# Kernel optimization log

Measured on AMD Instinct MI355X. Metric: run time of the kernel, lower is better.

## Reference

```python
import jax, jax.numpy as jnp
import numpy as np

HEADS = 12
HEAD_DIM = 64          # dim_out // heads = 768 // 12
Q_STRIDE = 4
WINDOW_SIZE = 16       # post-pool tokens per window; pre-pool = Q_STRIDE*WINDOW_SIZE = 64
DIM = 768
DIM_OUT = 768


def setup_inputs() -> dict:
    key = jax.random.key(0)
    k1, k2, k3 = jax.random.split(key, 3)
    B, N = 32, 3136
    x = jax.random.normal(k1, (B, N, DIM), dtype=jnp.float32)
    Wqkv = jax.random.normal(k2, (DIM, 3 * DIM_OUT), dtype=jnp.float32) * 0.02
    bqkv = jnp.zeros((3 * DIM_OUT,), dtype=jnp.float32)
    Wproj = jax.random.normal(k3, (DIM_OUT, DIM_OUT), dtype=jnp.float32) * 0.02
    bproj = jnp.zeros((DIM_OUT,), dtype=jnp.float32)
    return {"x": x, "Wqkv": Wqkv, "bqkv": bqkv, "Wproj": Wproj, "bproj": bproj}


def reference(x, Wqkv, bqkv, Wproj, bproj):
    B, N, _ = x.shape
    num_windows = N // (Q_STRIDE * WINDOW_SIZE)  # 49
    scale = HEAD_DIM ** (-0.5)

    # QKV projection (torch Linear uses x @ W^T; here Wqkv is stored [dim, 3*dim_out])
    qkv = x @ Wqkv + bqkv                                  # [B, N, 3*dim_out]
    # Same reshape as torch: windows are the inner split of the token axis
    qkv = qkv.reshape(B, N // num_windows, num_windows, 3, HEADS, HEAD_DIM)
    qkv = jnp.transpose(qkv, (3, 0, 4, 2, 1, 5))           # [3, B, h, w, t, d]
    q, k, v = qkv[0], qkv[1], qkv[2]                       # t = Q_STRIDE*WINDOW_SIZE

    # Query max-pooling over stride groups
    q = q.reshape(B, HEADS, num_windows, Q_STRIDE, WINDOW_SIZE, HEAD_DIM).max(axis=3)
    # q: [B, h, w, WINDOW_SIZE, d]

    # Scaled dot-product attention within each window
    logits = jnp.einsum('bhwqd,bhwkd->bhwqk', q, k) * scale
    attn = jax.nn.softmax(logits, axis=-1)
    o = jnp.einsum('bhwqk,bhwkd->bhwqd', attn, v)          # [B, h, w, q, d]

    # transpose(1,3) then flatten tokens, channels = heads*head_dim
    o = jnp.transpose(o, (0, 3, 2, 1, 4)).reshape(B, -1, DIM_OUT)
    return o @ Wproj + bproj
```

## Files before the change

kernel.cpp:

```cpp
#include <hip/hip_runtime.h>
#include <hip/hip_bf16.h>


typedef __bf16 bf16x8 __attribute__((ext_vector_type(8)));
typedef float f32x4 __attribute__((ext_vector_type(4)));
typedef unsigned short u16x8 __attribute__((ext_vector_type(8)));

#define GLOBAL_AS __attribute__((address_space(1)))
#define LDS_AS __attribute__((address_space(3)))

__device__ __forceinline__ unsigned short f2bf(float f) {
    unsigned u = __builtin_bit_cast(unsigned, f);
    u += 0x7FFFu + ((u >> 16) & 1u);
    return (unsigned short)(u >> 16);
}
__device__ __forceinline__ float bf2f(unsigned short h) {
    return __builtin_bit_cast(float, (unsigned)h << 16);
}

__device__ __forceinline__ void load16_to_lds(const void* g, void* l) {
    __builtin_amdgcn_global_load_lds((const GLOBAL_AS unsigned int*)g,
                                     (LDS_AS unsigned int*)l, 16, 0, 0);
}

__global__ void cvt_f32_bf16(const float* __restrict__ in,
                             unsigned short* __restrict__ out, long n4) {
    long i = (long)blockIdx.x * blockDim.x + threadIdx.x;
    if (i >= n4) return;
    float4 f = ((const float4*)in)[i];
    uint2 u;
    u.x = (unsigned)f2bf(f.x) | ((unsigned)f2bf(f.y) << 16);
    u.y = (unsigned)f2bf(f.z) | ((unsigned)f2bf(f.w) << 16);
    ((uint2*)out)[i] = u;
}

__global__ void transpose_cvt(const float* __restrict__ W,
                              unsigned short* __restrict__ Wt, int K, int N) {
    __shared__ float tile[32][33];
    int bx = blockIdx.x * 32;
    int by = blockIdx.y * 32;
    int tx = threadIdx.x & 31, ty = threadIdx.x >> 5;
    #pragma unroll
    for (int i = 0; i < 32; i += 8)
        tile[ty + i][tx] = W[(size_t)(by + ty + i) * N + bx + tx];
    __syncthreads();
    #pragma unroll
    for (int i = 0; i < 32; i += 8)
        Wt[(size_t)(bx + ty + i) * K + by + tx] = f2bf(tile[tx][ty + i]);
}

template <bool OUT_BF16>
__global__ __launch_bounds__(256)
void gemm_bt(const unsigned short* __restrict__ A,
             const unsigned short* __restrict__ Bt,
             const float* __restrict__ bias,
             void* __restrict__ Cv, int M, int N, int K) {
    __shared__ alignas(16) unsigned short lsA[128 * 64];
    __shared__ alignas(16) unsigned short lsB[128 * 64];

    const int tid  = threadIdx.x;
    const int lane = tid & 63;
    const int wave = tid >> 6;
    const int wm = (wave >> 1) * 64;
    const int wn = (wave & 1) * 64;

    const int nwg = (int)(gridDim.x * gridDim.y);
    const int hid = (int)(blockIdx.y * gridDim.x + blockIdx.x);
    int lid = hid;
    if ((nwg & 7) == 0) {
        const int cpx = nwg >> 3;
        lid = (hid & 7) * cpx + (hid >> 3);
    }
    const int tileX = lid % (int)gridDim.x;
    const int tileY = lid / (int)gridDim.x;
    const long bm = (long)tileY * 128;
    const long bn = (long)tileX * 128;

    const int arow  = tid >> 3;
    const int acolb = (((tid & 7) ^ ((tid >> 3) & 7)) * 16);
    const char* gA = (const char*)A + ((bm + arow) * (long)K) * 2 + acolb;
    const char* gB = (const char*)Bt + ((bn + arow) * (long)K) * 2 + acolb;
    const long rowStep = (long)K * 2 * 32;
    const int ldsWaveBase = wave * 512;

    f32x4 acc[4][4] = {};

    for (int kt = 0; kt < K; kt += 64) {
        #pragma unroll
        for (int it = 0; it < 4; ++it) {
            load16_to_lds(gA + it * rowStep, &lsA[it * 2048 + ldsWaveBase]);
            load16_to_lds(gB + it * rowStep, &lsB[it * 2048 + ldsWaveBase]);
        }
        gA += 128; gB += 128;
        __syncthreads();
        #pragma unroll
        for (int ks = 0; ks < 64; ks += 32) {
            bf16x8 af[4], bg[4];
            const int colSwz = (ks + ((lane >> 4) & 3) * 8) ^ ((lane & 7) * 8);
            #pragma unroll
            for (int i = 0; i < 4; ++i) {
                const int rowA = wm + i * 16 + (lane & 15);
                af[i] = *(const bf16x8*)&lsA[rowA * 64 + colSwz];
                const int rowB = wn + i * 16 + (lane & 15);
                bg[i] = *(const bf16x8*)&lsB[rowB * 64 + colSwz];
            }
            #pragma unroll
            for (int i = 0; i < 4; ++i)
                #pragma unroll
                for (int j = 0; j < 4; ++j)
                    acc[i][j] = __builtin_amdgcn_mfma_f32_16x16x32_bf16(
                        bg[j], af[i], acc[i][j], 0, 0, 0);
        }
        __syncthreads();
    }

    const int lane15 = lane & 15;
    const int quad   = lane >> 4;
    const long rbase = bm + wm + lane15;
    const int  cbase = (int)bn + wn + quad * 4;
    #pragma unroll
    for (int j = 0; j < 4; ++j) {
        const int col = cbase + j * 16;
        const float4 bv = *(const float4*)&bias[col];
        #pragma unroll
        for (int i = 0; i < 4; ++i) {
            const long row = rbase + i * 16;
            const size_t idx = (size_t)row * N + col;
            const float v0 = acc[i][j][0] + bv.x;
            const float v1 = acc[i][j][1] + bv.y;
            const float v2 = acc[i][j][2] + bv.z;
            const float v3 = acc[i][j][3] + bv.w;
            if constexpr (OUT_BF16) {
                ushort4 s;
                s.x = f2bf(v0); s.y = f2bf(v1); s.z = f2bf(v2); s.w = f2bf(v3);
                *(ushort4*)((unsigned short*)Cv + idx) = s;
            } else {
                float4 s;
                s.x = v0; s.y = v1; s.z = v2; s.w = v3;
                *(float4*)((float*)Cv + idx) = s;
            }
        }
    }
}

__global__ __launch_bounds__(256)
void attn_win_mfma(const unsigned short* __restrict__ qkv,
                   unsigned short* __restrict__ o) {
    const int hg = blockIdx.x;
    const int w  = blockIdx.y;
    const int b  = blockIdx.z;
    const int wave = threadIdx.x >> 6;
    const int lane = threadIdx.x & 63;
    const int h = hg * 4 + wave;
    const int l = lane & 15;
    const int quad = lane >> 4;

    __shared__ alignas(16) unsigned short vT[4][64 * 72];
    __shared__ alignas(16) unsigned short ps[4][16 * 72];

    const long tokStride = 49L * 2304;
    const long base = ((long)b * 3136 + w) * 2304 + h * 64;

    bf16x8 af[2];
    {
        const unsigned short* qr = qkv + base + (long)l * tokStride + quad * 8;
        float m0[8], m1[8];
        #pragma unroll
        for (int sg = 0; sg < 4; ++sg) {
            uint4 u0 = *(const uint4*)(qr + (long)sg * 16 * tokStride);
            uint4 u1 = *(const uint4*)(qr + (long)sg * 16 * tokStride + 32);
            const unsigned short* p0 = (const unsigned short*)&u0;
            const unsigned short* p1 = (const unsigned short*)&u1;
            #pragma unroll
            for (int e = 0; e < 8; ++e) {
                float f0 = bf2f(p0[e]), f1 = bf2f(p1[e]);
                if (sg == 0) { m0[e] = f0; m1[e] = f1; }
                else { m0[e] = fmaxf(m0[e], f0); m1[e] = fmaxf(m1[e], f1); }
            }
        }
        u16x8 a0, a1;
        #pragma unroll
        for (int e = 0; e < 8; ++e) {
            a0[e] = f2bf(m0[e] * 0.125f);
            a1[e] = f2bf(m1[e] * 0.125f);
        }
        af[0] = __builtin_bit_cast(bf16x8, a0);
        af[1] = __builtin_bit_cast(bf16x8, a1);
    }

    {
        const unsigned short* vr = qkv + base + (long)lane * tokStride + 1536;
        unsigned short* vw = &vT[wave][0];
        #pragma unroll
        for (int i = 0; i < 8; ++i) {
            uint4 u = *(const uint4*)(vr + i * 8);
            const unsigned short* pe = (const unsigned short*)&u;
            #pragma unroll
            for (int e = 0; e < 8; ++e)
                vw[(i * 8 + e) * 72 + lane] = pe[e];
        }
    }

    f32x4 Sc[4] = {};
    {
        bf16x8 bk0, bk1;
        #pragma unroll
        for (int tt = 0; tt < 4; ++tt) {
            const unsigned short* kr =
                qkv + base + (long)(tt * 16 + l) * tokStride + 768 + quad * 8;
            bk0 = __builtin_bit_cast(bf16x8, *(const uint4*)kr);
            bk1 = __builtin_bit_cast(bf16x8, *(const uint4*)(kr + 32));
            Sc[tt] = __builtin_amdgcn_mfma_f32_16x16x32_bf16(af[0], bk0, Sc[tt], 0, 0, 0);
            Sc[tt] = __builtin_amdgcn_mfma_f32_16x16x32_bf16(af[1], bk1, Sc[tt], 0, 0, 0);
        }
    }

    float pr[4][4];
    {
        #pragma unroll
        for (int r = 0; r < 4; ++r) {
            float mx = fmaxf(fmaxf(Sc[0][r], Sc[1][r]), fmaxf(Sc[2][r], Sc[3][r]));
            #pragma unroll
            for (int off = 1; off < 16; off <<= 1)
                mx = fmaxf(mx, __shfl_xor(mx, off));
            float sum = 0.f;
            #pragma unroll
            for (int tt = 0; tt < 4; ++tt) {
                pr[tt][r] = __expf(Sc[tt][r] - mx);
                sum += pr[tt][r];
            }
            #pragma unroll
            for (int off = 1; off < 16; off <<= 1)
                sum += __shfl_xor(sum, off);
            const float inv = 1.0f / sum;
            #pragma unroll
            for (int tt = 0; tt < 4; ++tt) pr[tt][r] *= inv;
        }
    }

    {
        unsigned short* pw = &ps[wave][0];
        #pragma unroll
        for (int r = 0; r < 4; ++r)
            #pragma unroll
            for (int tt = 0; tt < 4; ++tt)
                pw[(quad * 4 + r) * 72 + tt * 16 + l] = f2bf(pr[tt][r]);
    }

    f32x4 Oc[4] = {};
    {
        #pragma unroll
        for (int s = 0; s < 2; ++s) {
            bf16x8 ap = *(const bf16x8*)&ps[wave][l * 72 + s * 32 + quad * 8];
            #pragma unroll
            for (int tt = 0; tt < 4; ++tt) {
                bf16x8 bv = *(const bf16x8*)&vT[wave][(tt * 16 + l) * 72 + s * 32 + quad * 8];
                Oc[tt] = __builtin_amdgcn_mfma_f32_16x16x32_bf16(ap, bv, Oc[tt], 0, 0, 0);
            }
        }
    }

    {
        const long obase = ((long)b * 784 + (long)(quad * 4) * 49 + w) * 768 + h * 64 + l;
        #pragma unroll
        for (int tt = 0; tt < 4; ++tt)
            #pragma unroll
            for (int r = 0; r < 4; ++r)
                o[obase + (long)r * 49 * 768 + tt * 16] = f2bf(Oc[tt][r]);
    }
}

extern "C" void kernel_launch(void* const* d_in, const int* in_sizes, int n_in,
                              void* d_out, int out_size, void* d_ws, size_t ws_size,
                              hipStream_t stream) {
    const float* x     = (const float*)d_in[0];
    const float* Wqkv  = (const float*)d_in[1];
    const float* bqkv  = (const float*)d_in[2];
    const float* Wproj = (const float*)d_in[3];
    const float* bproj = (const float*)d_in[4];
    float* out = (float*)d_out;

    const long needed1 = (32L * 3136 * 768 + 32L * 3136 * 2304 +
                          25088L * 768 + 2304L * 768 + 768L * 768) * 2;
    const int C  = (ws_size >= (size_t)needed1) ? 1 : 4;
    const int CB = 32 / C;
    const long XC = (long)CB * 3136 * 768;
    const long QC = (long)CB * 3136 * 2304;

    char* p = (char*)d_ws;
    unsigned short* xb    = (unsigned short*)p; p += XC * 2;
    unsigned short* qkvb  = (unsigned short*)p; p += QC * 2;
    unsigned short* ob    = (unsigned short*)p; p += 25088L * 768 * 2;
    unsigned short* WqkvT = (unsigned short*)p; p += 2304L * 768 * 2;
    unsigned short* WprojT= (unsigned short*)p; p += 768L * 768 * 2;

    transpose_cvt<<<dim3(72, 24), 256, 0, stream>>>(Wqkv, WqkvT, 768, 2304);
    transpose_cvt<<<dim3(24, 24), 256, 0, stream>>>(Wproj, WprojT, 768, 768);

    const int M = CB * 3136;
    for (int c = 0; c < C; ++c) {
        cvt_f32_bf16<<<(int)(XC / 4 / 256), 256, 0, stream>>>(x + (size_t)c * XC, xb, XC / 4);
        gemm_bt<true><<<dim3(18, M / 128), 256, 0, stream>>>(
            xb, WqkvT, bqkv, qkvb, M, 2304, 768);
        attn_win_mfma<<<dim3(3, 49, CB), 256, 0, stream>>>(
            qkvb, ob + (size_t)c * CB * 784 * 768);
    }
    gemm_bt<false><<<dim3(6, 196), 256, 0, stream>>>(
        ob, WprojT, bproj, out, 25088, 768, 768);
}
```

Measured before the change: 1.230 ms.

## Enlarge GEMM tiles to 256x256 with double-buffered LDS prefetch

Both GEMMs now use 256x256 block tiles with 512 threads (8 waves, each computing 128x64) instead of 128x128 tiles with 256 threads. LDS is double-buffered so the next K-tile's global-to-LDS loads are issued while the current tile is being consumed, leaving one barrier per K step. The XCD-aware block remap now also handles grid sizes that are not multiples of 8. The larger tiles raise operand reuse and cut global traffic per FLOP. The cost is 128 KB of LDS and a 128-register accumulator per thread, which limits occupancy and leaves fewer blocks to fill the GPU.

Result: faster. 1.178 ms (-4.3%).

```diff
diff --git a/kernel.cpp b/kernel.cpp
--- a/kernel.cpp
+++ b/kernel.cpp
@@ -50,72 +50,80 @@
 }
 
 template <bool OUT_BF16>
-__global__ __launch_bounds__(256)
-void gemm_bt(const unsigned short* __restrict__ A,
-             const unsigned short* __restrict__ Bt,
-             const float* __restrict__ bias,
-             void* __restrict__ Cv, int M, int N, int K) {
-    __shared__ alignas(16) unsigned short lsA[128 * 64];
-    __shared__ alignas(16) unsigned short lsB[128 * 64];
+__global__ __launch_bounds__(512, 2)
+void gemm_bt256(const unsigned short* __restrict__ A,
+                const unsigned short* __restrict__ Bt,
+                const float* __restrict__ bias,
+                void* __restrict__ Cv, int M, int N, int K) {
+    __shared__ alignas(16) unsigned short lsA[2][256 * 64];
+    __shared__ alignas(16) unsigned short lsB[2][256 * 64];
 
     const int tid  = threadIdx.x;
     const int lane = tid & 63;
     const int wave = tid >> 6;
-    const int wm = (wave >> 1) * 64;
-    const int wn = (wave & 1) * 64;
+    const int wm = (wave >> 2) * 128;
+    const int wn = (wave & 3) * 64;
 
     const int nwg = (int)(gridDim.x * gridDim.y);
     const int hid = (int)(blockIdx.y * gridDim.x + blockIdx.x);
-    int lid = hid;
-    if ((nwg & 7) == 0) {
-        const int cpx = nwg >> 3;
-        lid = (hid & 7) * cpx + (hid >> 3);
-    }
+    const int q8  = nwg >> 3, r8 = nwg & 7;
+    const int xcd = hid & 7;
+    const int lid = (xcd < r8 ? xcd * (q8 + 1) : r8 * (q8 + 1) + (xcd - r8) * q8)
+                    + (hid >> 3);
     const int tileX = lid % (int)gridDim.x;
     const int tileY = lid / (int)gridDim.x;
-    const long bm = (long)tileY * 128;
-    const long bn = (long)tileX * 128;
+    const long bm = (long)tileY * 256;
+    const long bn = (long)tileX * 256;
 
     const int arow  = tid >> 3;
-    const int acolb = (((tid & 7) ^ ((tid >> 3) & 7)) * 16);
+    const int acolb = (((tid & 7) ^ (arow & 7)) * 16);
     const char* gA = (const char*)A + ((bm + arow) * (long)K) * 2 + acolb;
     const char* gB = (const char*)Bt + ((bn + arow) * (long)K) * 2 + acolb;
-    const long rowStep = (long)K * 2 * 32;
+    const long rowStep = (long)K * 2 * 64;
     const int ldsWaveBase = wave * 512;
 
-    f32x4 acc[4][4] = {};
-
-    for (int kt = 0; kt < K; kt += 64) {
+    f32x4 acc[8][4] = {};
+
+    const int NT = K >> 6;
+
+    auto STAGE = [&](int buf, int t) {
+        const char* a = gA + (long)t * 128;
+        const char* b = gB + (long)t * 128;
         #pragma unroll
         for (int it = 0; it < 4; ++it) {
-            load16_to_lds(gA + it * rowStep, &lsA[it * 2048 + ldsWaveBase]);
-            load16_to_lds(gB + it * rowStep, &lsB[it * 2048 + ldsWaveBase]);
-        }
-        gA += 128; gB += 128;
+            load16_to_lds(a + it * rowStep, &lsA[buf][it * 4096 + ldsWaveBase]);
+            load16_to_lds(b + it * rowStep, &lsB[buf][it * 4096 + ldsWaveBase]);
+        }
+    };
+
+    STAGE(0, 0);
+    int cur = 0;
+    const int lane15 = lane & 15;
+    const int quad   = lane >> 4;
+
+    for (int t = 0; t < NT; ++t) {
         __syncthreads();
+        if (t + 1 < NT) STAGE(cur ^ 1, t + 1);
         #pragma unroll
         for (int ks = 0; ks < 64; ks += 32) {
-            bf16x8 af[4], bg[4];
-            const int colSwz = (ks + ((lane >> 4) & 3) * 8) ^ ((lane & 7) * 8);
-            #pragma unroll
-            for (int i = 0; i < 4; ++i) {
-                const int rowA = wm + i * 16 + (lane & 15);
-                af[i] = *(const bf16x8*)&lsA[rowA * 64 + colSwz];
-                const int rowB = wn + i * 16 + (lane & 15);
-                bg[i] = *(const bf16x8*)&lsB[rowB * 64 + colSwz];
-            }
-            #pragma unroll
-            for (int i = 0; i < 4; ++i)
+            bf16x8 af[8], bg[4];
+            const int colSwz = (ks + quad * 8) ^ ((lane & 7) * 8);
+            #pragma unroll
+            for (int i = 0; i < 8; ++i)
+                af[i] = *(const bf16x8*)&lsA[cur][(wm + i * 16 + lane15) * 64 + colSwz];
+            #pragma unroll
+            for (int j = 0; j < 4; ++j)
+                bg[j] = *(const bf16x8*)&lsB[cur][(wn + j * 16 + lane15) * 64 + colSwz];
+            #pragma unroll
+            for (int i = 0; i < 8; ++i)
                 #pragma unroll
                 for (int j = 0; j < 4; ++j)
                     acc[i][j] = __builtin_amdgcn_mfma_f32_16x16x32_bf16(
                         bg[j], af[i], acc[i][j], 0, 0, 0);
         }
-        __syncthreads();
-    }
-
-    const int lane15 = lane & 15;
-    const int quad   = lane >> 4;
+        cur ^= 1;
+    }
+
     const long rbase = bm + wm + lane15;
     const int  cbase = (int)bn + wn + quad * 4;
     #pragma unroll
@@ -123,7 +131,7 @@
         const int col = cbase + j * 16;
         const float4 bv = *(const float4*)&bias[col];
         #pragma unroll
-        for (int i = 0; i < 4; ++i) {
+        for (int i = 0; i < 8; ++i) {
             const long row = rbase + i * 16;
             const size_t idx = (size_t)row * N + col;
             const float v0 = acc[i][j][0] + bv.x;
@@ -300,11 +308,11 @@
     const int M = CB * 3136;
     for (int c = 0; c < C; ++c) {
         cvt_f32_bf16<<<(int)(XC / 4 / 256), 256, 0, stream>>>(x + (size_t)c * XC, xb, XC / 4);
-        gemm_bt<true><<<dim3(18, M / 128), 256, 0, stream>>>(
+        gemm_bt256<true><<<dim3(9, M / 256), 512, 0, stream>>>(
             xb, WqkvT, bqkv, qkvb, M, 2304, 768);
         attn_win_mfma<<<dim3(3, 49, CB), 256, 0, stream>>>(
             qkvb, ob + (size_t)c * CB * 784 * 768);
     }
-    gemm_bt<false><<<dim3(6, 196), 256, 0, stream>>>(
+    gemm_bt256<false><<<dim3(3, 98), 512, 0, stream>>>(
         ob, WprojT, bproj, out, 25088, 768, 768);
 }
```
